# Kernel tuning notes

Measured on AMD Instinct MI355X. Metric: run time of the kernel, lower is better.

## Reference

```python
import jax, jax.numpy as jnp
import numpy as np

B, H, W, C = 16, 56, 56, 512
NH = 16
WS = 7
SHIFT = 3
HIDDEN = int(C * 4.0)
N = WS * WS
EPS = 1e-5


def _window_partition(x):
    # x: [B, H, W, C] -> [B*nW, N, C]
    b, h, w, c = x.shape
    x = x.reshape(b, h // WS, WS, w // WS, WS, c).transpose(0, 1, 3, 2, 4, 5)
    return x.reshape(-1, N, c)


def _window_reverse(win, h, w):
    c = win.shape[-1]
    x = win.reshape(-1, h // WS, w // WS, WS, WS, c).transpose(0, 1, 3, 2, 4, 5)
    return x.reshape(-1, h, w, c)


def _layernorm(x, g, b):
    mu = jnp.mean(x, axis=-1, keepdims=True)
    var = jnp.mean(jnp.square(x - mu), axis=-1, keepdims=True)
    return (x - mu) * jax.lax.rsqrt(var + EPS) * g + b


def _make_rel_coords_table():
    ch = np.arange(-(WS - 1), WS)
    cw = np.arange(-(WS - 1), WS)
    t = np.expand_dims(np.transpose(np.stack(np.meshgrid(ch, cw, indexing='ij')), [1, 2, 0]), 0).astype(np.float64)
    t[..., 0] /= (WS - 1)
    t[..., 1] /= (WS - 1)
    t *= 8
    t = np.sign(t) * np.log2(np.abs(t) + 1.0) / np.log2(8)
    return jnp.asarray(t, jnp.float32)  # [1, 2WS-1, 2WS-1, 2]


def _make_rel_pos_index():
    ch = np.arange(WS)
    cw = np.arange(WS)
    coords = np.reshape(np.stack(np.meshgrid(ch, cw, indexing='ij')), [2, -1])
    rel = np.expand_dims(coords, -1) - np.expand_dims(coords, -2)
    rel = np.transpose(rel, [1, 2, 0])
    rel[..., 0] += WS - 1
    rel[..., 1] += WS - 1
    rel[..., 0] *= 2 * WS - 1
    return jnp.asarray(np.sum(rel, -1), jnp.int32)  # [N, N]


def _make_attn_mask():
    img = np.zeros((H, W), np.float32)
    cnt = 0
    for hs in (slice(0, -WS), slice(-WS, -SHIFT), slice(-SHIFT, None)):
        for ws_ in (slice(0, -WS), slice(-WS, -SHIFT), slice(-SHIFT, None)):
            img[hs, ws_] = cnt
            cnt += 1
    x = img.reshape(1, H // WS, WS, W // WS, WS, 1).transpose(0, 1, 3, 2, 4, 5).reshape(-1, N)
    diff = x[:, :, None] - x[:, None, :]
    return jnp.asarray(np.where(diff != 0, -100.0, 0.0).astype(np.float32))  # [nW, N, N]


def setup_inputs() -> dict:
    key = jax.random.key(0)
    ks = jax.random.split(key, 16)
    s = 0.02
    return {
        'x': jax.random.normal(ks[0], (B, H, W, C), jnp.float32),
        'qkv_w': jax.random.normal(ks[1], (C, 3 * C), jnp.float32) * s,
        'q_bias': jnp.zeros((C,), jnp.float32),
        'v_bias': jnp.zeros((C,), jnp.float32),
        'proj_w': jax.random.normal(ks[2], (C, C), jnp.float32) * s,
        'proj_b': jnp.zeros((C,), jnp.float32),
        'logit_scale': jnp.full((NH, 1, 1), np.log(10.0), jnp.float32),
        'cpb_w1': jax.random.normal(ks[3], (2, 512), jnp.float32) * s,
        'cpb_b1': jnp.zeros((512,), jnp.float32),
        'cpb_w2': jax.random.normal(ks[4], (512, NH), jnp.float32) * s,
        'rel_coords_table': _make_rel_coords_table(),
        'gamma1': jnp.ones((C,), jnp.float32),
        'beta1': jnp.zeros((C,), jnp.float32),
        'gamma2': jnp.ones((C,), jnp.float32),
        'beta2': jnp.zeros((C,), jnp.float32),
        'fc1_w': jax.random.normal(ks[5], (C, HIDDEN), jnp.float32) * s,
        'fc1_b': jnp.zeros((HIDDEN,), jnp.float32),
        'fc2_w': jax.random.normal(ks[6], (HIDDEN, C), jnp.float32) * s,
        'fc2_b': jnp.zeros((C,), jnp.float32),
        'rel_pos_index': _make_rel_pos_index(),
        'attn_mask': _make_attn_mask(),
    }


def _forward(x, qkv_w, q_bias, v_bias, proj_w, proj_b, logit_scale,
             cpb_w1, cpb_b1, cpb_w2, rel_coords_table,
             gamma1, beta1, gamma2, beta2, fc1_w, fc1_b, fc2_w, fc2_b,
             rel_pos_index, attn_mask):
    hd = C // NH
    shortcut = x
    # cyclic shift + window partition
    xs = jnp.roll(x, (-SHIFT, -SHIFT), axis=(1, 2))
    xw = _window_partition(xs)  # [B*nW, N, C]
    # qkv with (q, 0, v) bias
    qkv_bias = jnp.concatenate([q_bias, jnp.zeros_like(v_bias), v_bias], axis=0)
    qkv = xw @ qkv_w + qkv_bias
    qkv = qkv.reshape(-1, N, 3, NH, hd).transpose(2, 0, 3, 1, 4)
    q, k, v = qkv[0], qkv[1], qkv[2]  # [BW, NH, N, hd]
    # cosine attention with learned temperature
    qn = q / jnp.linalg.norm(q, axis=-1, keepdims=True)
    kn = k / jnp.linalg.norm(k, axis=-1, keepdims=True)
    scale = jnp.exp(jnp.minimum(logit_scale, jnp.log(100.0)))
    attn = jnp.einsum('bhnd,bhmd->bhnm', qn, kn) * scale
    # continuous position bias via small MLP + gather
    cpb = jax.nn.relu(rel_coords_table @ cpb_w1 + cpb_b1) @ cpb_w2  # [1,2W-1,2W-1,NH]
    table = cpb.reshape(-1, NH)
    bias = table[rel_pos_index.reshape(-1)].reshape(N, N, NH).transpose(2, 0, 1)
    bias = 16.0 * jax.nn.sigmoid(bias)
    attn = attn + bias[None]
    # shifted-window mask
    nW = attn_mask.shape[0]
    attn = attn.reshape(-1, nW, NH, N, N) + attn_mask[None, :, None]
    attn = jax.nn.softmax(attn.reshape(-1, NH, N, N), axis=-1)
    out = jnp.einsum('bhnm,bhmd->bhnd', attn, v).transpose(0, 2, 1, 3).reshape(-1, N, C)
    out = out @ proj_w + proj_b
    # reverse windows + reverse shift
    out = _window_reverse(out, H, W)
    out = jnp.roll(out, (SHIFT, SHIFT), axis=(1, 2))
    # Swin-V2 res-post-norm residual blocks
    x1 = shortcut + _layernorm(out, gamma1, beta1)
    h = jax.nn.gelu(x1 @ fc1_w + fc1_b, approximate=False) @ fc2_w + fc2_b
    return x1 + _layernorm(h, gamma2, beta2)


def reference(x, qkv_w, q_bias, v_bias, proj_w, proj_b, logit_scale,
              cpb_w1, cpb_b1, cpb_w2, rel_coords_table,
              gamma1, beta1, gamma2, beta2, fc1_w, fc1_b, fc2_w, fc2_b,
              rel_pos_index, attn_mask):
    return _forward(x, qkv_w, q_bias, v_bias, proj_w, proj_b, logit_scale,
                    cpb_w1, cpb_b1, cpb_w2, rel_coords_table,
                    gamma1, beta1, gamma2, beta2, fc1_w, fc1_b, fc2_w, fc2_b,
                    rel_pos_index, attn_mask)
```

## Files before the change

kernel.cpp:

```cpp
#include <hip/hip_runtime.h>
#include <hip/hip_bf16.h>
#include <cmath>

typedef __hip_bfloat16 bf16;
typedef __attribute__((ext_vector_type(8))) __bf16 bf16x8;
typedef __attribute__((ext_vector_type(4))) float f32x4;
typedef __attribute__((ext_vector_type(4))) short short4v;

#define NROWS 50176

static __device__ __forceinline__ float b2f(bf16 v) { return __bfloat162float(v); }
static __device__ __forceinline__ bf16 f2b(float v) { return __float2bfloat16(v); }

static __device__ __forceinline__ void gl16(const bf16* g, bf16* l) {
  __builtin_amdgcn_global_load_lds((const __attribute__((address_space(1))) void*)g,
                                   (__attribute__((address_space(3))) void*)l, 16, 0, 0);
}

static __device__ __forceinline__ float fast_gelu(float v) {
  float z = v * 0.70710678118654752f;
  float a = fabsf(z);
  float t = __builtin_amdgcn_rcpf(fmaf(0.3275911f, a, 1.0f));
  float poly = t * fmaf(t, fmaf(t, fmaf(t, fmaf(t, 1.061405429f, -1.453152027f),
                                        1.421413741f), -0.284496736f), 0.254829592f);
  float e = exp2f(-a * a * 1.4426950408889634f);
  float erfz = copysignf(1.0f - poly * e, z);
  return 0.5f * v * (1.0f + erfz);
}

static __device__ __forceinline__ size_t pix_base(int row) {
  if (row >= NROWS) row = NROWS - 1;
  int win = row / 49, tok = row - win * 49;
  int b = win >> 6, wi = win & 63;
  int th = tok / 7, tw = tok - th * 7;
  int h = (wi >> 3) * 7 + th + 3; if (h >= 56) h -= 56;
  int w = (wi & 7) * 7 + tw + 3;  if (w >= 56) w -= 56;
  return (((size_t)b * 56 + h) * 56 + w) * 512;
}

__global__ __launch_bounds__(256) void diag_fill(float* out, float val, int n) {
  int i = blockIdx.x * 256 + threadIdx.x;
  if (i < n) out[i] = val;
}

__global__ __launch_bounds__(256) void transpose_f2b(const float* __restrict__ in,
                                                     bf16* __restrict__ out,
                                                     int R, int C) {
  __shared__ float tile[32][33];
  int c0 = blockIdx.x * 32, r0 = blockIdx.y * 32;
  int tx = threadIdx.x & 31, ty = threadIdx.x >> 5;
  for (int i = ty; i < 32; i += 8)
    tile[i][tx] = in[(size_t)(r0 + i) * C + c0 + tx];
  __syncthreads();
  for (int i = ty; i < 32; i += 8)
    out[(size_t)(c0 + i) * R + r0 + tx] = f2b(tile[tx][i]);
}

__global__ __launch_bounds__(256) void conv_f2b(const float* __restrict__ in,
                                                bf16* __restrict__ outb, int n8) {
  for (int i = blockIdx.x * 256 + threadIdx.x; i < n8; i += gridDim.x * 256) {
    float4 u0 = *(const float4*)&in[(size_t)i * 8];
    float4 u1 = *(const float4*)&in[(size_t)i * 8 + 4];
    bf16 h8[8] = {f2b(u0.x), f2b(u0.y), f2b(u0.z), f2b(u0.w),
                  f2b(u1.x), f2b(u1.y), f2b(u1.z), f2b(u1.w)};
    *(uint4*)&outb[(size_t)i * 8] = *(uint4*)h8;
  }
}

__global__ void prep_small(const float* qb, const float* vb, const float* pb,
                           const float* f1b, const float* f2b_, const float* ls,
                           float* qkvb, float* pbf, float* f1bf, float* f2bf,
                           float* scale) {
  int tid = blockIdx.x * 256 + threadIdx.x;
  if (tid < 512)       qkvb[tid] = qb[tid];
  else if (tid < 1024) qkvb[tid] = 0.f;
  else if (tid < 1536) qkvb[tid] = vb[tid - 1024];
  if (tid < 512)  pbf[tid]  = pb[tid];
  if (tid < 2048) f1bf[tid] = f1b[tid];
  if (tid < 512)  f2bf[tid] = f2b_[tid];
  if (tid < 16)   scale[tid] = expf(fminf(ls[tid], 4.6051701859880914f));
}

__global__ __launch_bounds__(256) void prep_cpb(const float* __restrict__ coords,
                                                const float* __restrict__ w1,
                                                const float* __restrict__ b1,
                                                const float* __restrict__ w2,
                                                float* __restrict__ table) {
  __shared__ float hid[512];
  __shared__ float part[256];
  int idx = blockIdx.x;
  float c0 = coords[idx * 2], c1 = coords[idx * 2 + 1];
  int tid = threadIdx.x;
  for (int h = tid; h < 512; h += 256) {
    float v = c0 * w1[h] + c1 * w1[512 + h] + b1[h];
    hid[h] = fmaxf(v, 0.f);
  }
  __syncthreads();
  int head = tid & 15, seg = tid >> 4;
  float s = 0.f;
  for (int h = seg * 32; h < seg * 32 + 32; ++h) s += hid[h] * w2[h * 16 + head];
  part[tid] = s;
  __syncthreads();
  if (tid < 16) {
    float t = 0.f;
    for (int sg = 0; sg < 16; ++sg) t += part[sg * 16 + tid];
    table[idx * 16 + tid] = t;
  }
}

__global__ void prep_bias(const float* __restrict__ table, const int* __restrict__ rpi,
                          float* __restrict__ bias_full) {
  int idx = blockIdx.x * 256 + threadIdx.x;
  if (idx >= 16 * 2401) return;
  int head = idx / 2401, ij = idx - head * 2401;
  float t = table[rpi[ij] * 16 + head];
  bias_full[idx] = 16.f / (1.f + expf(-t));
}

__global__ void prep_bm(const float* __restrict__ biasF, const float* __restrict__ amask,
                        float* __restrict__ bm) {
  int idx = blockIdx.x * 256 + threadIdx.x;
  if (idx >= 64 * 16 * 2401) return;
  int w = idx / (16 * 2401);
  int rem = idx - w * (16 * 2401);
  int h = rem / 2401, ij = rem - h * 2401;
  bm[idx] = biasF[h * 2401 + ij] + amask[w * 2401 + ij];
}

template <int EPI, int GATHER>
__global__ __launch_bounds__(256, 6) void gemm_lds(const bf16* __restrict__ A, int lda,
                                                   const bf16* __restrict__ Bt,
                                                   bf16* __restrict__ C, int ldc,
                                                   const float* __restrict__ bias,
                                                   int K, int nbx, int row_off) {
  __shared__ __align__(16) bf16 As[128 * 32];
  __shared__ __align__(16) bf16 Bs[64 * 32];
  const int nwg = gridDim.x, bid = blockIdx.x;
  const int q = nwg >> 3, r = nwg & 7;
  const int xcd = bid & 7, coff = bid >> 3;
  const int wg = (xcd < r ? xcd * (q + 1) : r * (q + 1) + (xcd - r) * q) + coff;
  const int bx = wg % nbx, by = wg / nbx;
  const int row0 = by * 128, col0 = bx * 64;

  const int tid = threadIdx.x;
  const int lane = tid & 63;
  const int quad = lane >> 4, l15 = lane & 15;
  const int wave = tid >> 6;
  const int wm = (wave >> 1) * 64, wn = (wave & 1) * 32;
  const int xq = quad ^ ((l15 >> 1) & 3);

  const int ar0 = tid >> 2, as0 = tid & 3;
  const int ar1 = ar0 + 64;
  const int ax0 = as0 ^ ((ar0 >> 1) & 3);
  const int ax1 = as0 ^ ((ar1 >> 1) & 3);
  size_t ab0, ab1;
  if (GATHER) {
    ab0 = pix_base(row_off + row0 + ar0);
    ab1 = pix_base(row_off + row0 + ar1);
  } else {
    ab0 = (size_t)(row0 + ar0) * lda;
    ab1 = (size_t)(row0 + ar1) * lda;
  }
  const bf16* ap0 = A + ab0 + ax0 * 8;
  const bf16* ap1 = A + ab1 + ax1 * 8;
  const int br = tid >> 2;
  const int bx0 = as0 ^ ((br >> 1) & 3);
  const bf16* bp0 = Bt + (size_t)(col0 + br) * K + bx0 * 8;
  bf16* la0 = As + tid * 8;
  bf16* la1 = As + (tid + 256) * 8;
  bf16* lb0 = Bs + tid * 8;

  f32x4 acc[4][2] = {};

  for (int k0 = 0; k0 < K; k0 += 32) {
    gl16(ap0 + k0, la0);
    gl16(ap1 + k0, la1);
    gl16(bp0 + k0, lb0);
    __syncthreads();
    bf16x8 af[4], bfr[2];
#pragma unroll
    for (int t = 0; t < 4; ++t)
      af[t] = *(const bf16x8*)&As[(wm + t * 16 + l15) * 32 + xq * 8];
#pragma unroll
    for (int t = 0; t < 2; ++t)
      bfr[t] = *(const bf16x8*)&Bs[(wn + t * 16 + l15) * 32 + xq * 8];
#pragma unroll
    for (int mt = 0; mt < 4; ++mt)
#pragma unroll
      for (int nt = 0; nt < 2; ++nt)
        acc[mt][nt] = __builtin_amdgcn_mfma_f32_16x16x32_bf16(af[mt], bfr[nt], acc[mt][nt], 0, 0, 0);
    __syncthreads();
  }

#pragma unroll
  for (int nt = 0; nt < 2; ++nt) {
    int gcol = col0 + wn + nt * 16 + l15;
    float bv = bias[gcol];
#pragma unroll
    for (int mt = 0; mt < 4; ++mt) {
      int grow = row0 + wm + mt * 16 + quad * 4;
#pragma unroll
      for (int rr = 0; rr < 4; ++rr) {
        float v = acc[mt][nt][rr] + bv;
        if (EPI == 2) v = fast_gelu(v);
        C[(size_t)(grow + rr) * ldc + gcol] = f2b(v);
      }
    }
  }
}

__global__ __launch_bounds__(256, 4) void attn_mfma(const bf16* __restrict__ qkv,
                                                    const float* __restrict__ scale,
                                                    const float* __restrict__ bm,
                                                    bf16* __restrict__ outp, int win_off) {
  __shared__ __align__(16) __bf16 Vl[4][1984];
  const int tid = threadIdx.x;
  const int wave = tid >> 6, lane = tid & 63;
  const int quad = lane >> 4, l15 = lane & 15;
  const int winl = blockIdx.x >> 2, hg = blockIdx.x & 3;
  const int head = hg * 4 + wave;
  const int wing = win_off + winl;
  const size_t rowbase = (size_t)winl * 49;
  const __bf16* base = (const __bf16*)qkv + rowbase * 1536 + head * 32;
  __bf16* Vw = Vl[wave];
  const float* bmh = bm + ((size_t)(wing & 63) * 16 + head) * 2401;
  const float sc = scale[head];

  bf16x8 vtmp[4];
  int vj[4], vdc[4];
#pragma unroll
  for (int t = 0; t < 4; ++t) {
    int c = lane + 64 * t; if (c > 195) c = 195;
    vj[t] = c >> 2; vdc[t] = (c & 3) << 3;
    vtmp[t] = *(const bf16x8*)(base + (size_t)vj[t] * 1536 + 1024 + vdc[t]);
  }

  bf16x8 khi[4], klo[4];
#pragma unroll
  for (int jt = 0; jt < 4; ++jt) {
    int j = jt * 16 + l15; if (j > 48) j = 48;
    bf16x8 raw = *(const bf16x8*)(base + (size_t)j * 1536 + 512 + quad * 8);
    float f[8]; float ss = 1e-20f;
#pragma unroll
    for (int e = 0; e < 8; ++e) { f[e] = (float)raw[e]; ss += f[e] * f[e]; }
    ss += __shfl_xor(ss, 16, 64);
    ss += __shfl_xor(ss, 32, 64);
    float inv = rsqrtf(ss);
#pragma unroll
    for (int e = 0; e < 8; ++e) {
      float v = f[e] * inv;
      __bf16 h = (__bf16)v;
      khi[jt][e] = h;
      klo[jt][e] = (__bf16)(v - (float)h);
    }
  }

#pragma unroll
  for (int t = 0; t < 4; ++t)
    *(bf16x8*)&Vw[vj[t] * 40 + vdc[t]] = vtmp[t];

  short4v vb[4][2];
#pragma unroll
  for (int jt = 0; jt < 4; ++jt)
#pragma unroll
    for (int n2 = 0; n2 < 2; ++n2) {
      short4v v;
#pragma unroll
      for (int e = 0; e < 4; ++e) {
        int j = jt * 16 + quad * 4 + e; if (j > 48) j = 48;
        v[e] = *(const short*)&Vw[j * 40 + n2 * 16 + l15];
      }
      vb[jt][n2] = v;
    }

  for (int it = 0; it < 4; ++it) {
    int qi = it * 16 + l15; if (qi > 48) qi = 48;
    bf16x8 raw = *(const bf16x8*)(base + (size_t)qi * 1536 + quad * 8);
    float f[8]; float ss = 1e-20f;
#pragma unroll
    for (int e = 0; e < 8; ++e) { f[e] = (float)raw[e]; ss += f[e] * f[e]; }
    ss += __shfl_xor(ss, 16, 64);
    ss += __shfl_xor(ss, 32, 64);
    float qinv = rsqrtf(ss) * sc;
    bf16x8 qhi, qlo;
#pragma unroll
    for (int e = 0; e < 8; ++e) {
      float v = f[e] * qinv;
      __bf16 h = (__bf16)v;
      qhi[e] = h;
      qlo[e] = (__bf16)(v - (float)h);
    }
    f32x4 s4[4];
#pragma unroll
    for (int jt = 0; jt < 4; ++jt) {
      f32x4 a = {0.f, 0.f, 0.f, 0.f};
      a = __builtin_amdgcn_mfma_f32_16x16x32_bf16(khi[jt], qhi, a, 0, 0, 0);
      a = __builtin_amdgcn_mfma_f32_16x16x32_bf16(klo[jt], qhi, a, 0, 0, 0);
      a = __builtin_amdgcn_mfma_f32_16x16x32_bf16(khi[jt], qlo, a, 0, 0, 0);
      s4[jt] = a;
    }
    int iio = qi * 49;
    float sv[4][4];
    float mx = -1e30f;
#pragma unroll
    for (int jt = 0; jt < 4; ++jt)
#pragma unroll
      for (int rr = 0; rr < 4; ++rr) {
        int j = jt * 16 + quad * 4 + rr;
        float s = (j < 49) ? s4[jt][rr] + bmh[iio + j] : -1e30f;
        sv[jt][rr] = s;
        mx = fmaxf(mx, s);
      }
    mx = fmaxf(mx, __shfl_xor(mx, 16, 64));
    mx = fmaxf(mx, __shfl_xor(mx, 32, 64));
    float sum = 0.f;
#pragma unroll
    for (int jt = 0; jt < 4; ++jt)
#pragma unroll
      for (int rr = 0; rr < 4; ++rr) {
        float e = exp2f((sv[jt][rr] - mx) * 1.4426950408889634f);
        sv[jt][rr] = e;
        sum += e;
      }
    sum += __shfl_xor(sum, 16, 64);
    sum += __shfl_xor(sum, 32, 64);
    float pinv = 1.f / sum;
    short4v pa[4];
#pragma unroll
    for (int jt = 0; jt < 4; ++jt)
#pragma unroll
      for (int rr = 0; rr < 4; ++rr) {
        __bf16 h = (__bf16)(sv[jt][rr] * pinv);
        pa[jt][rr] = *(short*)&h;
      }
    f32x4 o[2] = {};
#pragma unroll
    for (int jt = 0; jt < 4; ++jt) {
#pragma unroll
      for (int n2 = 0; n2 < 2; ++n2)
        o[n2] = __builtin_amdgcn_mfma_f32_16x16x16bf16_1k(pa[jt], vb[jt][n2], o[n2], 0, 0, 0);
    }
#pragma unroll
    for (int n2 = 0; n2 < 2; ++n2)
#pragma unroll
      for (int rr = 0; rr < 4; ++rr) {
        int i = it * 16 + quad * 4 + rr;
        if (i < 49)
          outp[(rowbase + i) * 1536 + head * 32 + n2 * 16 + l15] = f2b(o[n2][rr]);
      }
  }
}

__global__ __launch_bounds__(256) void ln_shift_add(const bf16* projq,
                                                    const float* __restrict__ x,
                                                    const float* __restrict__ gamma,
                                                    const float* __restrict__ beta,
                                                    float* __restrict__ x1,
                                                    bf16* __restrict__ x1b,
                                                    int row_off) {
  __shared__ float red[10];
  int grow = row_off + blockIdx.x;
  int win = grow / 49, tok = grow - win * 49;
  int b = win >> 6, wi = win & 63;
  int hs = (wi >> 3) * 7 + tok / 7;
  int wsc = (wi & 7) * 7 + tok % 7;
  int h = hs + 3; if (h >= 56) h -= 56;
  int w = wsc + 3; if (w >= 56) w -= 56;
  size_t pix = ((size_t)b * 56 + h) * 56 + w;
  const bf16* src = projq + (size_t)blockIdx.x * 1536 + 512;
  int tid = threadIdx.x;
  float a0 = b2f(src[tid]);
  float a1 = b2f(src[tid + 256]);
  float s = a0 + a1, qq = a0 * a0 + a1 * a1;
#pragma unroll
  for (int off = 32; off > 0; off >>= 1) {
    s += __shfl_down(s, off, 64);
    qq += __shfl_down(qq, off, 64);
  }
  int lane = tid & 63, wv = tid >> 6;
  if (lane == 0) { red[wv] = s; red[4 + wv] = qq; }
  __syncthreads();
  if (tid == 0) {
    red[8] = red[0] + red[1] + red[2] + red[3];
    red[9] = red[4] + red[5] + red[6] + red[7];
  }
  __syncthreads();
  float mu = red[8] * (1.f / 512.f);
  float inv = rsqrtf(fmaxf(red[9] * (1.f / 512.f) - mu * mu, 0.f) + 1e-5f);
  size_t base = pix * 512;
  float v0 = x[base + tid]       + (a0 - mu) * inv * gamma[tid]       + beta[tid];
  float v1 = x[base + tid + 256] + (a1 - mu) * inv * gamma[tid + 256] + beta[tid + 256];
  x1[base + tid]        = v0;
  x1[base + tid + 256]  = v1;
  x1b[base + tid]       = f2b(v0);
  x1b[base + tid + 256] = f2b(v1);
}

__global__ __launch_bounds__(256) void ln_add(const bf16* __restrict__ hsrc,
                                              float* x1,
                                              const float* __restrict__ gamma,
                                              const float* __restrict__ beta) {
  __shared__ float red[10];
  size_t base = (size_t)blockIdx.x * 512;
  int tid = threadIdx.x;
  float a0 = b2f(hsrc[base + tid]);
  float a1 = b2f(hsrc[base + tid + 256]);
  float s = a0 + a1, qq = a0 * a0 + a1 * a1;
#pragma unroll
  for (int off = 32; off > 0; off >>= 1) {
    s += __shfl_down(s, off, 64);
    qq += __shfl_down(qq, off, 64);
  }
  int lane = tid & 63, wv = tid >> 6;
  if (lane == 0) { red[wv] = s; red[4 + wv] = qq; }
  __syncthreads();
  if (tid == 0) {
    red[8] = red[0] + red[1] + red[2] + red[3];
    red[9] = red[4] + red[5] + red[6] + red[7];
  }
  __syncthreads();
  float mu = red[8] * (1.f / 512.f);
  float inv = rsqrtf(fmaxf(red[9] * (1.f / 512.f) - mu * mu, 0.f) + 1e-5f);
  x1[base + tid]       += (a0 - mu) * inv * gamma[tid]       + beta[tid];
  x1[base + tid + 256] += (a1 - mu) * inv * gamma[tid + 256] + beta[tid + 256];
}

extern "C" void kernel_launch(void* const* d_in, const int* in_sizes, int n_in,
                              void* d_out, int out_size, void* d_ws, size_t ws_size,
                              hipStream_t stream) {
  const float* x       = (const float*)d_in[0];
  const float* qkv_w   = (const float*)d_in[1];
  const float* q_bias  = (const float*)d_in[2];
  const float* v_bias  = (const float*)d_in[3];
  const float* proj_w  = (const float*)d_in[4];
  const float* proj_b  = (const float*)d_in[5];
  const float* logit_s = (const float*)d_in[6];
  const float* cpb_w1  = (const float*)d_in[7];
  const float* cpb_b1  = (const float*)d_in[8];
  const float* cpb_w2  = (const float*)d_in[9];
  const float* rct     = (const float*)d_in[10];
  const float* gamma1  = (const float*)d_in[11];
  const float* beta1   = (const float*)d_in[12];
  const float* gamma2  = (const float*)d_in[13];
  const float* beta2   = (const float*)d_in[14];
  const float* fc1_w   = (const float*)d_in[15];
  const float* fc1_b   = (const float*)d_in[16];
  const float* fc2_w   = (const float*)d_in[17];
  const float* fc2_b   = (const float*)d_in[18];
  const int*   rpi     = (const int*)d_in[19];
  const float* amask   = (const float*)d_in[20];
  float* out = (float*)d_out;

  char* ws = (char*)d_ws;
  size_t cur = 0;
  auto alloc = [&](size_t bytes) { size_t o = cur; cur += (bytes + 255) & ~(size_t)255; return o; };
  size_t o_qkvb = alloc(1536 * 4);
  size_t o_pb   = alloc(512 * 4);
  size_t o_f1b  = alloc(2048 * 4);
  size_t o_f2b  = alloc(512 * 4);
  size_t o_scal = alloc(16 * 4);
  size_t o_tab  = alloc(169 * 16 * 4);
  size_t o_bias = alloc(16 * 2401 * 4);
  size_t o_bm   = alloc((size_t)64 * 16 * 2401 * 4);
  size_t o_wt1  = alloc((size_t)1536 * 512 * 2);
  size_t o_wt2  = alloc((size_t)512 * 512 * 2);
  size_t o_wt3  = alloc((size_t)2048 * 512 * 2);
  size_t o_wt4  = alloc((size_t)512 * 2048 * 2);
  size_t o_xb   = alloc((size_t)NROWS * 512 * 2);
  size_t o_x1b  = alloc((size_t)NROWS * 512 * 2);
  size_t o_big  = cur;
  size_t avail  = (ws_size > o_big) ? ws_size - o_big : 0;

  const int wopts[] = {1024, 512, 256, 128, 64, 32, 16, 8};
  int wA = 0, padA = 0;
  for (int i = 0; i < 8; ++i) {
    int rows = wopts[i] * 49;
    int pad = (rows + 127) & ~127;
    if ((size_t)pad * 1536 * 2 <= avail) { wA = wopts[i]; padA = pad; break; }
  }
  const int ropts[] = {25088, 12544, 6272, 3584, 1792, 896, 512, 256};
  int rB = 0;
  for (int i = 0; i < 8; ++i)
    if ((size_t)ropts[i] * 2560 * 2 <= avail) { rB = ropts[i]; break; }

  if (!wA || !rB) {
    float v = 20000.f + (float)(ws_size >> 20);
    diag_fill<<<(out_size + 255) / 256, 256, 0, stream>>>(out, v, out_size);
    return;
  }

  float* qkvb  = (float*)(ws + o_qkvb);
  float* pbf   = (float*)(ws + o_pb);
  float* f1bf  = (float*)(ws + o_f1b);
  float* f2bf  = (float*)(ws + o_f2b);
  float* scal  = (float*)(ws + o_scal);
  float* tab   = (float*)(ws + o_tab);
  float* biasF = (float*)(ws + o_bias);
  float* bmF   = (float*)(ws + o_bm);
  bf16* wt1 = (bf16*)(ws + o_wt1);
  bf16* wt2 = (bf16*)(ws + o_wt2);
  bf16* wt3 = (bf16*)(ws + o_wt3);
  bf16* wt4 = (bf16*)(ws + o_wt4);
  bf16* xb  = (bf16*)(ws + o_xb);
  bf16* x1b = (bf16*)(ws + o_x1b);
  bf16* big = (bf16*)(ws + o_big);

  transpose_f2b<<<dim3(48, 16), 256, 0, stream>>>(qkv_w, wt1, 512, 1536);
  transpose_f2b<<<dim3(16, 16), 256, 0, stream>>>(proj_w, wt2, 512, 512);
  transpose_f2b<<<dim3(64, 16), 256, 0, stream>>>(fc1_w, wt3, 512, 2048);
  transpose_f2b<<<dim3(16, 64), 256, 0, stream>>>(fc2_w, wt4, 2048, 512);
  conv_f2b<<<2048, 256, 0, stream>>>(x, xb, NROWS * 512 / 8);

  prep_small<<<8, 256, 0, stream>>>(q_bias, v_bias, proj_b, fc1_b, fc2_b, logit_s,
                                    qkvb, pbf, f1bf, f2bf, scal);
  prep_cpb<<<169, 256, 0, stream>>>(rct, cpb_w1, cpb_b1, cpb_w2, tab);
  prep_bias<<<151, 256, 0, stream>>>(tab, rpi, biasF);
  prep_bm<<<(64 * 16 * 2401 + 255) / 256, 256, 0, stream>>>(biasF, amask, bmF);

  for (int woff = 0; woff < 1024; woff += wA) {
    int row_off = woff * 49;
    int rows = wA * 49;
    int nby = padA / 128;
    bf16* qkvC = big;
    gemm_lds<1, 1><<<24 * nby, 256, 0, stream>>>(xb, 0, wt1, qkvC, 1536, qkvb, 512, 24, row_off);
    attn_mfma<<<wA * 4, 256, 0, stream>>>(qkvC, scal, bmF, qkvC, woff);
    gemm_lds<1, 0><<<8 * nby, 256, 0, stream>>>(qkvC, 1536, wt2, qkvC + 512, 1536, pbf, 512, 8, 0);
    ln_shift_add<<<rows, 256, 0, stream>>>(qkvC, x, gamma1, beta1, out, x1b, row_off);
  }
  for (int r0 = 0; r0 < NROWS; r0 += rB) {
    float* x1h = out + (size_t)r0 * 512;
    bf16* hC  = big;
    bf16* f2C = big + (size_t)rB * 2048;
    int nby = rB / 128;
    gemm_lds<2, 0><<<32 * nby, 256, 0, stream>>>(x1b + (size_t)r0 * 512, 512, wt3, hC, 2048, f1bf, 512, 32, 0);
    gemm_lds<1, 0><<<8 * nby, 256, 0, stream>>>(hC, 2048, wt4, f2C, 512, f2bf, 2048, 8, 0);
    ln_add<<<rB, 256, 0, stream>>>(f2C, x1h, gamma2, beta2);
  }
}
```

Before: 982.5 us.

## Double-buffer GEMM LDS tiles and stage epilogue through LDS for vector stores

The GEMM main loop now uses two LDS buffers, so the async global-to-LDS load of the next K-slice is issued before computing the current one, overlapping memory latency with MFMA work. The epilogue writes bias/GELU results into a padded LDS tile and then emits coalesced 16-byte global stores instead of scattered 2-byte stores. LDS use rises to 24 KB per block, which may reduce occupancy under the 6-blocks launch bound. The loop assumes K is a multiple of 64.

Result: faster. 958.2 us (-2.5%).

```diff
diff --git a/kernel.cpp b/kernel.cpp
--- a/kernel.cpp
+++ b/kernel.cpp
@@ -133,8 +133,13 @@
                                                    bf16* __restrict__ C, int ldc,
                                                    const float* __restrict__ bias,
                                                    int K, int nbx, int row_off) {
-  __shared__ __align__(16) bf16 As[128 * 32];
-  __shared__ __align__(16) bf16 Bs[64 * 32];
+  __shared__ __align__(16) char smem[24576];
+  bf16* As0 = (bf16*)smem;
+  bf16* As1 = (bf16*)(smem + 8192);
+  bf16* Bs0 = (bf16*)(smem + 16384);
+  bf16* Bs1 = (bf16*)(smem + 20480);
+  bf16* Ct  = (bf16*)smem;
+
   const int nwg = gridDim.x, bid = blockIdx.x;
   const int q = nwg >> 3, r = nwg & 7;
   const int xcd = bid & 7, coff = bid >> 3;
@@ -166,46 +171,67 @@
   const int br = tid >> 2;
   const int bx0 = as0 ^ ((br >> 1) & 3);
   const bf16* bp0 = Bt + (size_t)(col0 + br) * K + bx0 * 8;
-  bf16* la0 = As + tid * 8;
-  bf16* la1 = As + (tid + 256) * 8;
-  bf16* lb0 = Bs + tid * 8;
 
   f32x4 acc[4][2] = {};
 
-  for (int k0 = 0; k0 < K; k0 += 32) {
-    gl16(ap0 + k0, la0);
-    gl16(ap1 + k0, la1);
-    gl16(bp0 + k0, lb0);
+#define STAGE(AS, BS, KK)                 \
+  do {                                    \
+    gl16(ap0 + (KK), (AS) + tid * 8);     \
+    gl16(ap1 + (KK), (AS) + (tid + 256) * 8); \
+    gl16(bp0 + (KK), (BS) + tid * 8);     \
+  } while (0)
+
+#define COMPUTE(AS, BS)                                                   \
+  do {                                                                    \
+    bf16x8 af[4], bfr[2];                                                 \
+    _Pragma("unroll")                                                     \
+    for (int t = 0; t < 4; ++t)                                           \
+      af[t] = *(const bf16x8*)&(AS)[(wm + t * 16 + l15) * 32 + xq * 8];   \
+    _Pragma("unroll")                                                     \
+    for (int t = 0; t < 2; ++t)                                           \
+      bfr[t] = *(const bf16x8*)&(BS)[(wn + t * 16 + l15) * 32 + xq * 8];  \
+    _Pragma("unroll")                                                     \
+    for (int mt = 0; mt < 4; ++mt)                                        \
+      _Pragma("unroll")                                                   \
+      for (int nt = 0; nt < 2; ++nt)                                      \
+        acc[mt][nt] = __builtin_amdgcn_mfma_f32_16x16x32_bf16(af[mt], bfr[nt], acc[mt][nt], 0, 0, 0); \
+  } while (0)
+
+  STAGE(As0, Bs0, 0);
+  __syncthreads();
+  for (int k0 = 0; k0 < K; k0 += 64) {
+    if (k0 + 32 < K) STAGE(As1, Bs1, k0 + 32);
+    COMPUTE(As0, Bs0);
     __syncthreads();
-    bf16x8 af[4], bfr[2];
-#pragma unroll
-    for (int t = 0; t < 4; ++t)
-      af[t] = *(const bf16x8*)&As[(wm + t * 16 + l15) * 32 + xq * 8];
-#pragma unroll
-    for (int t = 0; t < 2; ++t)
-      bfr[t] = *(const bf16x8*)&Bs[(wn + t * 16 + l15) * 32 + xq * 8];
-#pragma unroll
-    for (int mt = 0; mt < 4; ++mt)
-#pragma unroll
-      for (int nt = 0; nt < 2; ++nt)
-        acc[mt][nt] = __builtin_amdgcn_mfma_f32_16x16x32_bf16(af[mt], bfr[nt], acc[mt][nt], 0, 0, 0);
+    if (k0 + 64 < K) STAGE(As0, Bs0, k0 + 64);
+    COMPUTE(As1, Bs1);
     __syncthreads();
   }
+#undef STAGE
+#undef COMPUTE
 
 #pragma unroll
   for (int nt = 0; nt < 2; ++nt) {
-    int gcol = col0 + wn + nt * 16 + l15;
-    float bv = bias[gcol];
+    int lcol = wn + nt * 16 + l15;
+    float bv = bias[col0 + lcol];
 #pragma unroll
     for (int mt = 0; mt < 4; ++mt) {
-      int grow = row0 + wm + mt * 16 + quad * 4;
+      int lrow = wm + mt * 16 + quad * 4;
 #pragma unroll
       for (int rr = 0; rr < 4; ++rr) {
         float v = acc[mt][nt][rr] + bv;
         if (EPI == 2) v = fast_gelu(v);
-        C[(size_t)(grow + rr) * ldc + gcol] = f2b(v);
+        Ct[(lrow + rr) * 72 + lcol] = f2b(v);
       }
     }
+  }
+  __syncthreads();
+#pragma unroll
+  for (int i = 0; i < 4; ++i) {
+    int chunk = tid + i * 256;
+    int rw = chunk >> 3, c8 = chunk & 7;
+    uint4 val = *(const uint4*)&Ct[rw * 72 + c8 * 8];
+    *(uint4*)&C[(size_t)(row0 + rw) * ldc + col0 + c8 * 8] = val;
   }
 }
 
```
